# Kernel tuning notes

Measured on AMD Instinct MI355X. Metric: run time of the kernel, lower is better.

Reference implementation:

```python
import jax, jax.numpy as jnp
import numpy as np

REG = 0.1
PROX_ITERS = 5
SINK_ITERS = 100  # fixed-count stand-in for ot.sinkhorn's converged iteration
EPS = 1e-10
M_SAMPLES, N_SAMPLES, D_FEAT = 2048, 2048, 256


def sqdist(a, b):
    # ot.dist default: squared Euclidean pairwise distances, [na, nb]
    return (jnp.sum(a * a, axis=1)[:, None]
            + jnp.sum(b * b, axis=1)[None, :]
            - 2.0 * (a @ b.T))


def sinkhorn(p, q, M, reg, iters=SINK_ITERS):
    # classic scaling-iteration Sinkhorn (POT ot.sinkhorn semantics)
    K = jnp.exp(-M / reg)  # [n, m]
    u0 = jnp.ones_like(p) / p.shape[0]

    def step(u, _):
        v = q / (K.T @ u)
        u = p / (K @ v)
        return u, None

    u, _ = jax.lax.scan(step, u0, None, length=iters)
    v = q / (K.T @ u)
    return u[:, None] * K * v[None, :]


def sinkhorn_proximal(p, q, C, reg, n_iters):
    C = jax.lax.stop_gradient(C)  # torch: C.clone().detach()
    n, m = C.shape
    P0 = jnp.ones((n, m), C.dtype) / (n * m)

    def step(carry, _):
        P, _ = carry
        M = C - reg * jnp.log(P + EPS)
        M = M / jnp.max(M)
        P_new = sinkhorn(p, q, M, reg)
        return (P_new, P), None

    (P, P_pre), _ = jax.lax.scan(step, (P0, P0), None, length=n_iters)
    return jax.lax.stop_gradient(P), jax.lax.stop_gradient(P_pre)


def _divergence(T, C, reg):
    # M = normalized proximal cost; div = T @ M.T + reg * T @ (log(T)-1).T
    return T @ C.T + reg * (T @ (jnp.log(T + EPS) - 1.0).T)


def setup_inputs() -> dict:
    key = jax.random.key(0)
    kx, ky = jax.random.split(key)
    x = jax.random.normal(kx, (M_SAMPLES, D_FEAT), dtype=jnp.float32)
    y = jax.random.normal(ky, (N_SAMPLES, D_FEAT), dtype=jnp.float32)
    return {"x": x, "y": y}


def reference(x, y):
    reg = REG
    C_xx = sqdist(x, x)
    C_xy = sqdist(x, y)
    C_yy = sqdist(y, y)
    m = x.shape[0]
    n = y.shape[0]
    p_x = jnp.ones((m,), x.dtype) / m
    p_y = jnp.ones((n,), x.dtype) / n

    T_xx, T_xx_pre = sinkhorn_proximal(p_x, p_x, C_xx, reg, PROX_ITERS)
    T_xy, T_xy_pre = sinkhorn_proximal(p_x, p_y, C_xy, reg, PROX_ITERS)
    T_yy, T_yy_pre = sinkhorn_proximal(p_y, p_y, C_yy, reg, PROX_ITERS)

    M_xx = C_xx - reg * jnp.log(T_xx_pre + EPS)
    M_xx = M_xx / jnp.max(M_xx)
    M_xy = C_xy - reg * jnp.log(T_xy_pre + EPS)
    M_xy = M_xy / jnp.max(M_xy)
    M_yy = C_yy - reg * jnp.log(T_yy_pre + EPS)
    M_yy = M_yy / jnp.max(M_yy)

    cross_div = _divergence(T_xy, M_xy, reg)
    inner_div_x = _divergence(T_xx, M_xx, reg)
    inner_div_y = _divergence(T_yy, M_yy, reg)

    return cross_div.mean() - 0.5 * (inner_div_y.mean() + inner_div_x.mean())
```

## Files before the change

### kernel.cpp

```cpp
#include <hip/hip_runtime.h>
#include <hip/hip_fp16.h>
#include <math.h>

#define N 2048
#define D 256
#define NM (N*N)
#define REG 0.1f
#define EPSF 1e-10f
#define INV_N (1.0f/2048.0f)
#define P0CONST (1.0f/(2048.0f*2048.0f))
#define PROX 5
#define SINK 100
#define KSCALE 256.0f
#define TOL 1e-5f
#define SMEM_BYTES (131072 + 256)
#define SYS 64

__device__ __forceinline__ float waveReduceSum(float v){
#pragma unroll
    for(int o=32;o;o>>=1) v += __shfl_xor(v,o,64);
    return v;
}
__device__ __forceinline__ float waveReduceMax(float v){
#pragma unroll
    for(int o=32;o;o>>=1) v = fmaxf(v, __shfl_xor(v,o,64));
    return v;
}

__device__ __forceinline__ int swz(int c){
    return ((c>>3)&3)*512 + ((c>>5)<<3) + (c&7);
}

__global__ __launch_bounds__(256) void norms_k(const float* __restrict__ x,
                                               const float* __restrict__ y,
                                               float* __restrict__ nx,
                                               float* __restrict__ ny){
    const float* src = blockIdx.y ? y : x;
    float* dst       = blockIdx.y ? ny : nx;
    int w = threadIdx.x >> 6, lane = threadIdx.x & 63;
    int row = blockIdx.x*4 + w;
    const float4* r4 = (const float4*)(src + (size_t)row*D);
    float4 f = r4[lane];
    float s = f.x*f.x + f.y*f.y + f.z*f.z + f.w*f.w;
    s = waveReduceSum(s);
    if(lane==0) dst[row] = s;
}

__global__ __launch_bounds__(256) void sqdist_k(const float* __restrict__ x,
                                                const float* __restrict__ y,
                                                const float* __restrict__ nx,
                                                const float* __restrict__ ny,
                                                float* __restrict__ Cb){
    int mat = blockIdx.y;
    const float* A  = (mat<2)  ? x  : y;
    const float* B  = (mat==0) ? x  : y;
    const float* na = (mat<2)  ? nx : ny;
    const float* nb = (mat==0) ? nx : ny;
    float* Cm = Cb + (size_t)mat*NM;
    int bm = blockIdx.x >> 5, bn = blockIdx.x & 31;
    __shared__ float As[32][68];
    __shared__ float Bs[32][68];
    int tid = threadIdx.x;
    int tr = tid >> 4, tc = tid & 15;
    float acc[4][4] = {};
    for(int kb=0; kb<8; ++kb){
#pragma unroll
        for(int i=0;i<2;++i){
            int id = tid + 256*i;
            int r = id >> 3, c4 = id & 7;
            float4 a = *(const float4*)(A + (size_t)(bm*64 + r)*D + kb*32 + c4*4);
            As[c4*4+0][r]=a.x; As[c4*4+1][r]=a.y; As[c4*4+2][r]=a.z; As[c4*4+3][r]=a.w;
            float4 b = *(const float4*)(B + (size_t)(bn*64 + r)*D + kb*32 + c4*4);
            Bs[c4*4+0][r]=b.x; Bs[c4*4+1][r]=b.y; Bs[c4*4+2][r]=b.z; Bs[c4*4+3][r]=b.w;
        }
        __syncthreads();
#pragma unroll
        for(int d=0; d<32; ++d){
            float4 a = *(const float4*)&As[d][4*tr];
            float4 b = *(const float4*)&Bs[d][4*tc];
            acc[0][0] += a.x*b.x; acc[0][1] += a.x*b.y; acc[0][2] += a.x*b.z; acc[0][3] += a.x*b.w;
            acc[1][0] += a.y*b.x; acc[1][1] += a.y*b.y; acc[1][2] += a.y*b.z; acc[1][3] += a.y*b.w;
            acc[2][0] += a.z*b.x; acc[2][1] += a.z*b.y; acc[2][2] += a.z*b.z; acc[2][3] += a.z*b.w;
            acc[3][0] += a.w*b.x; acc[3][1] += a.w*b.y; acc[3][2] += a.w*b.z; acc[3][3] += a.w*b.w;
        }
        __syncthreads();
    }
    float nb0 = nb[bn*64 + tc*4 + 0];
    float nb1 = nb[bn*64 + tc*4 + 1];
    float nb2 = nb[bn*64 + tc*4 + 2];
    float nb3 = nb[bn*64 + tc*4 + 3];
#pragma unroll
    for(int i=0;i<4;++i){
        int row = bm*64 + tr*4 + i;
        float nr = na[row];
        float4 o;
        o.x = nr + nb0 - 2.0f*acc[i][0];
        o.y = nr + nb1 - 2.0f*acc[i][1];
        o.z = nr + nb2 - 2.0f*acc[i][2];
        o.w = nr + nb3 - 2.0f*acc[i][3];
        *(float4*)(Cm + (size_t)row*N + bn*64 + tc*4) = o;
    }
}

__global__ __launch_bounds__(1024) void coop_k(const float* __restrict__ C,
                                               float* __restrict__ Pa,
                                               float* __restrict__ Pb,
                                               float* __restrict__ ug,
                                               float* __restrict__ vg,
                                               float* __restrict__ maxsl,
                                               int* __restrict__ sync_){
    extern __shared__ char smem[];
    __half* Kl   = (__half*)smem;
    __half* KTl  = (__half*)(smem + 65536);
    float*  sRed = (float*)(smem + 131072);
    int*    sVote= (int*)(smem + 131072 + 64);

    const int tid = threadIdx.x;
    const int w = tid >> 6, lane = tid & 63;
    int bid = blockIdx.x;
    int m, nblk, row0, nrows;
    if(bid < 64)      { m=0; nblk=64;  nrows=32; row0=bid*32; }
    else if(bid <128) { m=2; nblk=64;  nrows=32; row0=(bid-64)*32; }
    else              { m=1; nblk=128; nrows=16; row0=(bid-128)*16; }
    int* SY0 = sync_ + m*5*SYS;
    int* SY1 = SY0 + SYS;
    int* SYG = SY0 + 2*SYS;
    int* SYC0= SY0 + 3*SYS;
    int* SYC1= SY0 + 4*SYS;
    const float* Cm = C + (size_t)m*NM;
    float* um = ug + m*N;
    float* vm = vg + m*N;
    const float lp0 = __logf(P0CONST + EPSF);
    int bcount = 0;

#define MATBAR() do{ \
    __syncthreads(); \
    if(tid==0){ \
        int* bc = (bcount&1) ? SY1 : SY0; \
        __threadfence(); \
        if(atomicAdd(bc,1)==nblk-1){ \
            atomicExch(bc,0); \
            __threadfence(); \
            atomicExch(SYG, bcount+1); \
        } else { \
            while(__hip_atomic_load(SYG, __ATOMIC_RELAXED, __HIP_MEMORY_SCOPE_AGENT) < bcount+1) \
                __builtin_amdgcn_s_sleep(1); \
            __threadfence(); \
        } \
    } \
    bcount++; \
    __syncthreads(); \
}while(0)

    auto halfstep = [&](const __half* S, const float* gin, float* gout, bool constU, bool vote){
        float4 ua[8];
        if(!constU){
            const float4* g4 = (const float4*)(gin + lane*32);
#pragma unroll
            for(int j=0;j<8;++j) ua[j]=g4[j];
        }
        const int rpw = (m==1)?1:2;
        for(int rr=0; rr<rpw; ++rr){
            int rl = w*rpw + rr;
            const float4* k4 = (const float4*)(S + (size_t)rl*2048);
            float s=0.f;
#pragma unroll
            for(int i=0;i<4;++i){
                float4 kb = k4[i*64+lane];
                const __half2* h=(const __half2*)&kb;
                float2 f0=__half22float2(h[0]),f1=__half22float2(h[1]),
                       f2=__half22float2(h[2]),f3=__half22float2(h[3]);
                if(constU) s += f0.x+f0.y+f1.x+f1.y+f2.x+f2.y+f3.x+f3.y;
                else s += f0.x*ua[2*i].x+f0.y*ua[2*i].y+f1.x*ua[2*i].z+f1.y*ua[2*i].w
                        + f2.x*ua[2*i+1].x+f2.y*ua[2*i+1].y+f3.x*ua[2*i+1].z+f3.y*ua[2*i+1].w;
            }
            s = waveReduceSum(s);
            if(constU) s *= INV_N;
            float nv = INV_N/s;
            if(lane==0){
                if(vote){
                    float ov = gout[row0+rl];
                    if(!(fabsf(nv-ov) <= TOL*nv)) sVote[0]=0;
                }
                gout[row0+rl] = nv;
            }
        }
    };

    for(int t=0; t<PROX; ++t){
        const float* Pin = (t&1) ? Pa : Pb;
        float*       Pout= (t&1) ? Pb : Pa;
        const float* Pm  = Pin + (size_t)m*NM;
        float mx = -1e30f;
        for(int r=0;r<nrows;++r){
            size_t base = (size_t)(row0+r)*N;
            float c0 = Cm[base+tid], c1 = Cm[base+tid+1024];
            float l0=lp0, l1=lp0;
            if(t){ l0=__logf(Pm[base+tid]+EPSF); l1=__logf(Pm[base+tid+1024]+EPSF); }
            mx = fmaxf(mx, fmaxf(c0-REG*l0, c1-REG*l1));
        }
        mx = waveReduceMax(mx);
        if(lane==0) sRed[w]=mx;
        __syncthreads();
        if(tid==0){
            float bm=sRed[0];
#pragma unroll
            for(int i=1;i<16;++i) bm=fmaxf(bm,sRed[i]);
            atomicMax((unsigned int*)&maxsl[m*SYS+t], __float_as_uint(bm));
            atomicExch(SYC0,0);
            atomicExch(SYC1,0);
        }
        MATBAR();
        float invmx = 1.0f / maxsl[m*SYS+t];
        for(int r=0;r<nrows;++r){
            size_t base=(size_t)(row0+r)*N;
#pragma unroll
            for(int h=0;h<2;++h){
                int c = tid + h*1024;
                float cc = Cm[base+c];
                float l = t ? __logf(Pm[base+c]+EPSF) : lp0;
                float Kv = __expf((cc-REG*l)*invmx*-10.0f)*KSCALE;
                Kl[r*2048 + swz(c)] = __float2half(Kv);
            }
        }
        if(m==1){
            for(int pass=0;pass<32;++pass){
                int i = pass*64 + (tid>>4); int jj = tid&15; int j = row0+jj;
                float cc = Cm[(size_t)i*N + j];
                float l = t ? __logf(Pm[(size_t)i*N+j]+EPSF) : lp0;
                float Kv = __expf((cc-REG*l)*invmx*-10.0f)*KSCALE;
                KTl[jj*2048 + swz(i)] = __float2half(Kv);
            }
        }
        __syncthreads();
        for(int it=0; it<SINK; ++it){
            halfstep((m==1)?KTl:Kl, um, vm, (t==0 && it==0), false);
            MATBAR();
            if(tid==0) sVote[0]=1;
            __syncthreads();
            halfstep(Kl, vm, um, false, true);
            __syncthreads();
            if(tid==0 && sVote[0] && it>=3) atomicAdd((it&1)?SYC1:SYC0,1);
            MATBAR();
            int cc = __hip_atomic_load((it&1)?SYC1:SYC0, __ATOMIC_RELAXED,
                                       __HIP_MEMORY_SCOPE_AGENT);
            if(tid==0) atomicExch((it&1)?SYC0:SYC1,0);
            if(cc==nblk) break;
        }
        halfstep((m==1)?KTl:Kl, um, vm, false, false);
        MATBAR();
        {
            float* Pom = Pout + (size_t)m*NM;
            for(int r=0;r<nrows;++r){
                size_t base=(size_t)(row0+r)*N;
                float uu = um[row0+r];
                float k0 = __half2float(Kl[r*2048+swz(tid)]);
                float k1 = __half2float(Kl[r*2048+swz(tid+1024)]);
                Pom[base+tid]      = uu*k0*vm[tid];
                Pom[base+tid+1024] = uu*k1*vm[tid+1024];
            }
        }
        MATBAR();
    }
#undef MATBAR
}

__global__ __launch_bounds__(256) void colsumM_k(const float* __restrict__ Cb,
                                                 const float* __restrict__ Pb,
                                                 const float* __restrict__ maxsl, int slot,
                                                 float* __restrict__ colM){
    int mat = blockIdx.y;
    const float4* C4 = (const float4*)(Cb + (size_t)mat*NM);
    const float4* P4 = (const float4*)(Pb + (size_t)mat*NM);
    float invmx = 1.0f / maxsl[mat*SYS + slot];
    int r0 = blockIdx.x*32;
    float4 a0 = {0,0,0,0}, a1 = {0,0,0,0};
    for(int r=0;r<32;++r){
        int base = (r0 + r)*512;
        {
            float4 c = C4[base + threadIdx.x]; float4 p = P4[base + threadIdx.x];
            a0.x += (c.x - REG*logf(p.x+EPSF))*invmx;
            a0.y += (c.y - REG*logf(p.y+EPSF))*invmx;
            a0.z += (c.z - REG*logf(p.z+EPSF))*invmx;
            a0.w += (c.w - REG*logf(p.w+EPSF))*invmx;
        }
        {
            float4 c = C4[base + 256 + threadIdx.x]; float4 p = P4[base + 256 + threadIdx.x];
            a1.x += (c.x - REG*logf(p.x+EPSF))*invmx;
            a1.y += (c.y - REG*logf(p.y+EPSF))*invmx;
            a1.z += (c.z - REG*logf(p.z+EPSF))*invmx;
            a1.w += (c.w - REG*logf(p.w+EPSF))*invmx;
        }
    }
    float* cm = colM + mat*N;
    atomicAdd(cm + 4*threadIdx.x + 0, a0.x);
    atomicAdd(cm + 4*threadIdx.x + 1, a0.y);
    atomicAdd(cm + 4*threadIdx.x + 2, a0.z);
    atomicAdd(cm + 4*threadIdx.x + 3, a0.w);
    atomicAdd(cm + 1024 + 4*threadIdx.x + 0, a1.x);
    atomicAdd(cm + 1024 + 4*threadIdx.x + 1, a1.y);
    atomicAdd(cm + 1024 + 4*threadIdx.x + 2, a1.z);
    atomicAdd(cm + 1024 + 4*threadIdx.x + 3, a1.w);
}

__global__ __launch_bounds__(256) void colsumTL_k(const float* __restrict__ Pb,
                                                  float* __restrict__ colT,
                                                  float* __restrict__ colL){
    int mat = blockIdx.y;
    const float4* P4 = (const float4*)(Pb + (size_t)mat*NM);
    int r0 = blockIdx.x*32;
    float4 t0 = {0,0,0,0}, t1 = {0,0,0,0};
    float4 l0 = {0,0,0,0}, l1 = {0,0,0,0};
    for(int r=0;r<32;++r){
        int base = (r0 + r)*512;
        {
            float4 p = P4[base + threadIdx.x];
            t0.x += p.x; t0.y += p.y; t0.z += p.z; t0.w += p.w;
            l0.x += logf(p.x+EPSF); l0.y += logf(p.y+EPSF);
            l0.z += logf(p.z+EPSF); l0.w += logf(p.w+EPSF);
        }
        {
            float4 p = P4[base + 256 + threadIdx.x];
            t1.x += p.x; t1.y += p.y; t1.z += p.z; t1.w += p.w;
            l1.x += logf(p.x+EPSF); l1.y += logf(p.y+EPSF);
            l1.z += logf(p.z+EPSF); l1.w += logf(p.w+EPSF);
        }
    }
    float* ct = colT + mat*N;
    float* cl = colL + mat*N;
    atomicAdd(ct + 4*threadIdx.x + 0, t0.x);
    atomicAdd(ct + 4*threadIdx.x + 1, t0.y);
    atomicAdd(ct + 4*threadIdx.x + 2, t0.z);
    atomicAdd(ct + 4*threadIdx.x + 3, t0.w);
    atomicAdd(ct + 1024 + 4*threadIdx.x + 0, t1.x);
    atomicAdd(ct + 1024 + 4*threadIdx.x + 1, t1.y);
    atomicAdd(ct + 1024 + 4*threadIdx.x + 2, t1.z);
    atomicAdd(ct + 1024 + 4*threadIdx.x + 3, t1.w);
    atomicAdd(cl + 4*threadIdx.x + 0, l0.x);
    atomicAdd(cl + 4*threadIdx.x + 1, l0.y);
    atomicAdd(cl + 4*threadIdx.x + 2, l0.z);
    atomicAdd(cl + 4*threadIdx.x + 3, l0.w);
    atomicAdd(cl + 1024 + 4*threadIdx.x + 0, l1.x);
    atomicAdd(cl + 1024 + 4*threadIdx.x + 1, l1.y);
    atomicAdd(cl + 1024 + 4*threadIdx.x + 2, l1.z);
    atomicAdd(cl + 1024 + 4*threadIdx.x + 3, l1.w);
}

__global__ __launch_bounds__(256) void final_k(const float* __restrict__ colM,
                                               const float* __restrict__ colT,
                                               const float* __restrict__ colL,
                                               float* __restrict__ out){
    __shared__ float red[8];
    __shared__ float divs[3];
    for(int mat=0; mat<3; ++mat){
        float s1=0.f, s2=0.f;
        for(int j=threadIdx.x; j<N; j+=256){
            float t = colT[mat*N+j];
            s1 += t * colM[mat*N+j];
            s2 += t * (colL[mat*N+j] - (float)N);
        }
        s1 = waveReduceSum(s1); s2 = waveReduceSum(s2);
        int w = threadIdx.x>>6, lane = threadIdx.x&63;
        if(lane==0){ red[w] = s1; red[4+w] = s2; }
        __syncthreads();
        if(threadIdx.x==0){
            float a = red[0]+red[1]+red[2]+red[3];
            float b = red[4]+red[5]+red[6]+red[7];
            divs[mat] = (a + REG*b) * (1.0f/((float)N*(float)N));
        }
        __syncthreads();
    }
    if(threadIdx.x==0) out[0] = divs[1] - 0.5f*(divs[0] + divs[2]);
}

extern "C" void kernel_launch(void* const* d_in, const int* in_sizes, int n_in,
                              void* d_out, int out_size, void* d_ws, size_t ws_size,
                              hipStream_t stream){
    const float* x = (const float*)d_in[0];
    const float* y = (const float*)d_in[1];
    float* ws = (float*)d_ws;
    float* C    = ws;
    float* Pa   = C  + (size_t)3*NM;
    float* Pb   = Pa + (size_t)3*NM;
    float* ug   = Pb + (size_t)3*NM;
    float* vg   = ug + 3*N;
    float* nx   = vg + 3*N;
    float* ny   = nx + N;
    float* zb   = ny + N;
    float* maxsl= zb;
    float* colM = zb + 3*SYS;
    float* colT = colM + 3*N;
    float* colL = colT + 3*N;
    int*   sync_= (int*)(colL + 3*N);
    size_t zbytes = ((size_t)3*SYS + 9*N)*sizeof(float) + (size_t)3*5*SYS*sizeof(int);
    hipMemsetAsync(zb, 0, zbytes, stream);

    norms_k <<<dim3(512,2), 256, 0, stream>>>(x, y, nx, ny);
    sqdist_k<<<dim3(1024,3),256, 0, stream>>>(x, y, nx, ny, C);

    hipFuncSetAttribute((const void*)coop_k,
                        hipFuncAttributeMaxDynamicSharedMemorySize, SMEM_BYTES);
    void* args[] = {(void*)&C, (void*)&Pa, (void*)&Pb, (void*)&ug, (void*)&vg,
                    (void*)&maxsl, (void*)&sync_};
    hipLaunchCooperativeKernel((void*)coop_k, dim3(256), dim3(1024),
                               args, SMEM_BYTES, stream);

    colsumM_k <<<dim3(64,3), 256, 0, stream>>>(C, Pb, maxsl, 4, colM);
    colsumTL_k<<<dim3(64,3), 256, 0, stream>>>(Pa, colT, colL);
    final_k   <<<1, 256, 0, stream>>>(colM, colT, colL, (float*)d_out);
}
```

Measured before the change: 1.552 ms.

## Rebuild proximal cost from on-chip K and scaling vectors, fuse convergence vote into barrier

```diff
diff --git a/kernel.cpp b/kernel.cpp
--- a/kernel.cpp
+++ b/kernel.cpp
@@ -12,7 +12,7 @@
 #define PROX 5
 #define SINK 100
 #define KSCALE 256.0f
-#define TOL 1e-5f
+#define TOL 4e-6f
 #define SMEM_BYTES (131072 + 256)
 #define SYS 64
 
@@ -125,32 +125,42 @@
     int* SY0 = sync_ + m*5*SYS;
     int* SY1 = SY0 + SYS;
     int* SYG = SY0 + 2*SYS;
-    int* SYC0= SY0 + 3*SYS;
-    int* SYC1= SY0 + 4*SYS;
     const float* Cm = C + (size_t)m*NM;
     float* um = ug + m*N;
     float* vm = vg + m*N;
     const float lp0 = __logf(P0CONST + EPSF);
     int bcount = 0;
 
-#define MATBAR() do{ \
-    __syncthreads(); \
-    if(tid==0){ \
-        int* bc = (bcount&1) ? SY1 : SY0; \
-        __threadfence(); \
-        if(atomicAdd(bc,1)==nblk-1){ \
-            atomicExch(bc,0); \
-            __threadfence(); \
-            atomicExch(SYG, bcount+1); \
-        } else { \
-            while(__hip_atomic_load(SYG, __ATOMIC_RELAXED, __HIP_MEMORY_SCOPE_AGENT) < bcount+1) \
-                __builtin_amdgcn_s_sleep(1); \
-            __threadfence(); \
-        } \
-    } \
-    bcount++; \
-    __syncthreads(); \
-}while(0)
+    auto MATBARV = [&](int wantVote)->int{
+        __syncthreads();
+        if(tid==0){
+            unsigned mv = wantVote ? (unsigned)sVote[0] : 0u;
+            unsigned* bc = (unsigned*)((bcount&1) ? SY1 : SY0);
+            int flag;
+            __threadfence();
+            unsigned old = atomicAdd(bc, 1u | (mv<<16));
+            if((old & 0xFFFFu) == (unsigned)(nblk-1)){
+                flag = (int)(((old>>16) + mv) == (unsigned)nblk);
+                atomicExch(bc, 0u);
+                __threadfence();
+                atomicExch(SYG, ((bcount+1)<<1) | flag);
+            } else {
+                int g;
+                for(;;){
+                    g = __hip_atomic_load(SYG, __ATOMIC_RELAXED, __HIP_MEMORY_SCOPE_AGENT);
+                    if((g>>1) >= bcount+1) break;
+                    __builtin_amdgcn_s_sleep(1);
+                }
+                __threadfence();
+                flag = g & 1;
+            }
+            sVote[1] = flag;
+            sVote[0] = 1;
+        }
+        bcount++;
+        __syncthreads();
+        return sVote[1];
+    };
 
     auto halfstep = [&](const __half* S, const float* gin, float* gout, bool constU, bool vote){
         float4 ua[8];
@@ -188,16 +198,26 @@
     };
 
     for(int t=0; t<PROX; ++t){
-        const float* Pin = (t&1) ? Pa : Pb;
-        float*       Pout= (t&1) ? Pb : Pa;
-        const float* Pm  = Pin + (size_t)m*NM;
+        float lv0=0.f, lv1=0.f, lvt=0.f;
+        if(t){
+            lv0 = __logf(vm[tid]);
+            lv1 = __logf(vm[tid+1024]);
+            if(m==1) lvt = __logf(vm[row0+(tid&15)]);
+        }
         float mx = -1e30f;
         for(int r=0;r<nrows;++r){
             size_t base = (size_t)(row0+r)*N;
             float c0 = Cm[base+tid], c1 = Cm[base+tid+1024];
-            float l0=lp0, l1=lp0;
-            if(t){ l0=__logf(Pm[base+tid]+EPSF); l1=__logf(Pm[base+tid+1024]+EPSF); }
-            mx = fmaxf(mx, fmaxf(c0-REG*l0, c1-REG*l1));
+            float m0, m1;
+            if(t==0){ m0 = c0 - REG*lp0; m1 = c1 - REG*lp0; }
+            else {
+                float lu = __logf(um[row0+r]);
+                float k0 = __half2float(Kl[r*2048+swz(tid)]);
+                float k1 = __half2float(Kl[r*2048+swz(tid+1024)]);
+                m0 = c0 - REG*(lu + lv0 + __logf(k0));
+                m1 = c1 - REG*(lu + lv1 + __logf(k1));
+            }
+            mx = fmaxf(mx, fmaxf(m0, m1));
         }
         mx = waveReduceMax(mx);
         if(lane==0) sRed[w]=mx;
@@ -207,50 +227,49 @@
 #pragma unroll
             for(int i=1;i<16;++i) bm=fmaxf(bm,sRed[i]);
             atomicMax((unsigned int*)&maxsl[m*SYS+t], __float_as_uint(bm));
-            atomicExch(SYC0,0);
-            atomicExch(SYC1,0);
-        }
-        MATBAR();
+        }
+        MATBARV(0);
         float invmx = 1.0f / maxsl[m*SYS+t];
         for(int r=0;r<nrows;++r){
             size_t base=(size_t)(row0+r)*N;
-#pragma unroll
-            for(int h=0;h<2;++h){
-                int c = tid + h*1024;
-                float cc = Cm[base+c];
-                float l = t ? __logf(Pm[base+c]+EPSF) : lp0;
-                float Kv = __expf((cc-REG*l)*invmx*-10.0f)*KSCALE;
-                Kl[r*2048 + swz(c)] = __float2half(Kv);
+            float lu = t ? __logf(um[row0+r]) : 0.f;
+            {
+                float c0 = Cm[base+tid];
+                float m0 = (t==0) ? (c0 - REG*lp0)
+                    : (c0 - REG*(lu + lv0 + __logf(__half2float(Kl[r*2048+swz(tid)]))));
+                Kl[r*2048+swz(tid)] = __float2half(__expf(m0*invmx*-10.0f)*KSCALE);
+                float c1 = Cm[base+tid+1024];
+                float m1 = (t==0) ? (c1 - REG*lp0)
+                    : (c1 - REG*(lu + lv1 + __logf(__half2float(Kl[r*2048+swz(tid+1024)]))));
+                Kl[r*2048+swz(tid+1024)] = __float2half(__expf(m1*invmx*-10.0f)*KSCALE);
             }
         }
         if(m==1){
             for(int pass=0;pass<32;++pass){
-                int i = pass*64 + (tid>>4); int jj = tid&15; int j = row0+jj;
-                float cc = Cm[(size_t)i*N + j];
-                float l = t ? __logf(Pm[(size_t)i*N+j]+EPSF) : lp0;
-                float Kv = __expf((cc-REG*l)*invmx*-10.0f)*KSCALE;
-                KTl[jj*2048 + swz(i)] = __float2half(Kv);
+                int i = pass*64 + (tid>>4); int jj = tid&15;
+                float cc = Cm[(size_t)i*N + row0 + jj];
+                float Mv;
+                if(t==0) Mv = cc - REG*lp0;
+                else {
+                    float lu = __logf(um[i]);
+                    float kp = __half2float(KTl[jj*2048+swz(i)]);
+                    Mv = cc - REG*(lu + lvt + __logf(kp));
+                }
+                KTl[jj*2048+swz(i)] = __float2half(__expf(Mv*invmx*-10.0f)*KSCALE);
             }
         }
         __syncthreads();
         for(int it=0; it<SINK; ++it){
             halfstep((m==1)?KTl:Kl, um, vm, (t==0 && it==0), false);
-            MATBAR();
-            if(tid==0) sVote[0]=1;
-            __syncthreads();
+            MATBARV(0);
             halfstep(Kl, vm, um, false, true);
-            __syncthreads();
-            if(tid==0 && sVote[0] && it>=3) atomicAdd((it&1)?SYC1:SYC0,1);
-            MATBAR();
-            int cc = __hip_atomic_load((it&1)?SYC1:SYC0, __ATOMIC_RELAXED,
-                                       __HIP_MEMORY_SCOPE_AGENT);
-            if(tid==0) atomicExch((it&1)?SYC0:SYC1,0);
-            if(cc==nblk) break;
+            int flag = MATBARV(it>=3);
+            if(flag) break;
         }
         halfstep((m==1)?KTl:Kl, um, vm, false, false);
-        MATBAR();
-        {
-            float* Pom = Pout + (size_t)m*NM;
+        MATBARV(0);
+        if(t>=3){
+            float* Pom = ((t&1) ? Pb : Pa) + (size_t)m*NM;
             for(int r=0;r<nrows;++r){
                 size_t base=(size_t)(row0+r)*N;
                 float uu = um[row0+r];
@@ -260,9 +279,7 @@
                 Pom[base+tid+1024] = uu*k1*vm[tid+1024];
             }
         }
-        MATBAR();
-    }
-#undef MATBAR
+    }
 }
 
 __global__ __launch_bounds__(256) void colsumM_k(const float* __restrict__ Cb,
```

Result: faster. 1.370 ms (-11.8%).
